# Performance work log

Measured on AMD Instinct MI355X. Metric: run time of the kernel, lower is better.

The kernel has to match this reference:

```python
import jax, jax.numpy as jnp
import numpy as np

B, S, D = 4, 4096, 1024
H, WIN = 16, 256
DK = D // H
NW = S // WIN


def setup_inputs() -> dict:
    key = jax.random.key(0)
    ks = jax.random.split(key, 11)
    mk = lambda k, shape: jax.random.normal(k, shape, dtype=jnp.float32)
    w = lambda k: mk(k, (D, D)) * 0.02  # torch Linear weight [out, in]
    b = lambda k: mk(k, (D,)) * 0.02
    return {
        "query": mk(ks[0], (B, S, D)),
        "key": mk(ks[1], (B, S, D)),
        "value": mk(ks[2], (B, S, D)),
        "Wq": w(ks[3]), "bq": b(ks[4]),
        "Wk": w(ks[5]), "bk": b(ks[6]),
        "Wv": w(ks[7]), "bv": b(ks[8]),
        "Wo": w(ks[9]), "bo": b(ks[10]),
    }


def reference(query, key, value, Wq, bq, Wk, bk, Wv, bv, Wo, bo):
    scale = 1.0 / float(DK) ** 0.5

    def proj(x, Wm, bi):
        y = x @ Wm.T + bi
        return y.reshape(B, S, H, DK).transpose(0, 2, 1, 3).reshape(B, H, NW, WIN, DK)

    q = proj(query, Wq, bq)
    k = proj(key, Wk, bk)
    v = proj(value, Wv, bv)

    scores = jnp.einsum("bhnqd,bhnkd->bhnqk", q, k) * scale
    p_attn = jax.nn.softmax(scores, axis=-1)
    x = jnp.einsum("bhnqk,bhnkd->bhnqd", p_attn, v)

    # merge windows + heads -> [B,S,D], then output projection
    x = x.reshape(B, H, S, DK).transpose(0, 2, 1, 3).reshape(B, S, D)
    return x @ Wo.T + bo
```

## Files before the change

kernel.cpp:

```cpp
#include <hip/hip_runtime.h>
#include <hip/hip_bf16.h>

typedef __attribute__((ext_vector_type(8))) __bf16 bf16x8;
typedef __attribute__((ext_vector_type(4))) float f32x4;

#define DEVI static __device__ __forceinline__


DEVI ushort f2bf(float f) {
  unsigned u = __builtin_bit_cast(unsigned, f);
  return (ushort)((u + 0x7fffu + ((u >> 16) & 1u)) >> 16);
}

union BF8 { unsigned u[4]; bf16x8 v; };

DEVI bf16x8 cvt8(const float* __restrict__ p) {
  const f32x4 a = *(const f32x4*)p;
  const f32x4 b = *(const f32x4*)(p + 4);
  BF8 r;
  asm("v_cvt_pk_bf16_f32 %0, %1, %2" : "=v"(r.u[0]) : "v"(a.x), "v"(a.y));
  asm("v_cvt_pk_bf16_f32 %0, %1, %2" : "=v"(r.u[1]) : "v"(a.z), "v"(a.w));
  asm("v_cvt_pk_bf16_f32 %0, %1, %2" : "=v"(r.u[2]) : "v"(b.x), "v"(b.y));
  asm("v_cvt_pk_bf16_f32 %0, %1, %2" : "=v"(r.u[3]) : "v"(b.z), "v"(b.w));
  return r.v;
}

DEVI bf16x8 cvt8r(f32x4 a, f32x4 b) {
  BF8 r;
  asm("v_cvt_pk_bf16_f32 %0, %1, %2" : "=v"(r.u[0]) : "v"(a.x), "v"(a.y));
  asm("v_cvt_pk_bf16_f32 %0, %1, %2" : "=v"(r.u[1]) : "v"(a.z), "v"(a.w));
  asm("v_cvt_pk_bf16_f32 %0, %1, %2" : "=v"(r.u[2]) : "v"(b.x), "v"(b.y));
  asm("v_cvt_pk_bf16_f32 %0, %1, %2" : "=v"(r.u[3]) : "v"(b.z), "v"(b.w));
  return r.v;
}

DEVI unsigned cvtpk1(float lo, float hi) {
  unsigned r;
  asm("v_cvt_pk_bf16_f32 %0, %1, %2" : "=v"(r) : "v"(lo), "v"(hi));
  return r;
}

DEVI void gload16(const void* g, void* l) {
  __builtin_amdgcn_global_load_lds(
      (const __attribute__((address_space(1))) unsigned*)g,
      (__attribute__((address_space(3))) unsigned*)l, 16, 0, 0);
}

DEVI int xcd_swizzle(int bid, int nwg) {
  return (bid & 7) * (nwg >> 3) + (bid >> 3);
}

DEVI f32x4 mfma16(bf16x8 a, bf16x8 b, f32x4 c) {
  return __builtin_amdgcn_mfma_f32_16x16x32_bf16(a, b, c, 0, 0, 0);
}


__global__ __launch_bounds__(256) void cvt_w(
    const float* __restrict__ wq, const float* __restrict__ wk,
    const float* __restrict__ wv, const float* __restrict__ wo,
    ushort* __restrict__ oq, ushort* __restrict__ ok2,
    ushort* __restrict__ ov, ushort* __restrict__ oo) {
  const int s = blockIdx.x >> 7;
  const int tb = blockIdx.x & 127;
  const float* src = s == 0 ? wq : (s == 1 ? wk : (s == 2 ? wv : wo));
  ushort* dst = s == 0 ? oq : (s == 1 ? ok2 : (s == 2 ? ov : oo));
  const unsigned G = 128 * 256;
  const unsigned t = tb * 256 + threadIdx.x;
#pragma unroll
  for (int j = 0; j < 4; ++j) {
    const size_t i = (size_t)t + (size_t)j * G;
    *(bf16x8*)(dst + i * 8) = cvt8(src + i * 8);
  }
}


template <int OUT>
__global__ __launch_bounds__(512, 2) void gemm_8ph(
    const ushort* __restrict__ A, const ushort* __restrict__ B,
    const float* __restrict__ bias, void* __restrict__ Cp, int N, int K) {
  __shared__ __align__(16) ushort Asm[4][8192];
  __shared__ __align__(16) ushort Bsm[4][8192];
  const int tid = threadIdx.x, lane = tid & 63;
  const int wv = tid >> 6;
  const int wr = wv >> 2, wc = wv & 3;
  const int cc = lane & 15, cr = lane >> 4;
  const int nw = N >> 8;
  const int work = xcd_swizzle(blockIdx.x, gridDim.x);
  const size_t m0 = (size_t)(work / nw) * 256;
  const size_t n0 = (size_t)(work % nw) * 256;

  const ushort *ag[2], *bg[2];
#pragma unroll
  for (int h = 0; h < 2; ++h) {
    const int u = tid + h * 512;
    const int row = u >> 2, slot = u & 3;
    const int gc = (slot ^ ((row >> 1) & 3)) * 8;
    ag[h] = A + (m0 + row) * (size_t)K + gc;
    bg[h] = B + (n0 + row) * (size_t)K + gc;
  }

  auto stageh = [&](int buf, int kt, int h) {
    gload16(ag[h] + kt, &Asm[buf][(tid + h * 512) * 8]);
    gload16(bg[h] + kt, &Bsm[buf][(tid + h * 512) * 8]);
  };

  f32x4 acc[8][4] = {};
  const int nt = K >> 5;

  int aoff[8], boff[4];
#pragma unroll
  for (int m = 0; m < 8; ++m) {
    const int row = wr * 128 + m * 16 + cc;
    aoff[m] = (row * 4 + (cr ^ ((row >> 1) & 3))) * 8;
  }
#pragma unroll
  for (int n = 0; n < 4; ++n) {
    const int row = wc * 64 + n * 16 + cc;
    boff[n] = (row * 4 + (cr ^ ((row >> 1) & 3))) * 8;
  }

#pragma unroll
  for (int p = 0; p < 3; ++p) {
    stageh(p, p << 5, 0);
    stageh(p, p << 5, 1);
  }
  asm volatile("s_waitcnt vmcnt(8)" ::: "memory");
  __builtin_amdgcn_s_barrier();
  asm volatile("" ::: "memory");

  for (int k = 0; k < nt; ++k) {
    const ushort* Ab = Asm[k & 3];
    const ushort* Bb = Bsm[k & 3];
    const int wb = (k + 3) & 3;
    const bool more = (k + 3 < nt);
    bf16x8 bf[4], af[4];

#pragma unroll
    for (int n = 0; n < 4; ++n) bf[n] = *(const bf16x8*)&Bb[boff[n]];
#pragma unroll
    for (int m = 0; m < 4; ++m) af[m] = *(const bf16x8*)&Ab[aoff[m]];
    if (more) stageh(wb, (k + 3) << 5, 0);
    __builtin_amdgcn_s_barrier();
    asm volatile("s_waitcnt lgkmcnt(0)" ::: "memory");
    __builtin_amdgcn_s_setprio(1);
#pragma unroll
    for (int m = 0; m < 4; ++m)
#pragma unroll
      for (int n = 0; n < 4; ++n)
        acc[m][n] = mfma16(af[m], bf[n], acc[m][n]);
    __builtin_amdgcn_s_setprio(0);
    asm volatile("" ::: "memory");
    __builtin_amdgcn_s_barrier();

#pragma unroll
    for (int m = 0; m < 4; ++m) af[m] = *(const bf16x8*)&Ab[aoff[4 + m]];
    if (more) stageh(wb, (k + 3) << 5, 1);
    if (k < nt - 3) {
      asm volatile("s_waitcnt vmcnt(8)" ::: "memory");
    } else if (k == nt - 3) {
      asm volatile("s_waitcnt vmcnt(4)" ::: "memory");
    } else if (k == nt - 2) {
      asm volatile("s_waitcnt vmcnt(0)" ::: "memory");
    }
    __builtin_amdgcn_s_barrier();
    asm volatile("s_waitcnt lgkmcnt(0)" ::: "memory");
    __builtin_amdgcn_s_setprio(1);
#pragma unroll
    for (int m = 0; m < 4; ++m)
#pragma unroll
      for (int n = 0; n < 4; ++n)
        acc[4 + m][n] = mfma16(af[m], bf[n], acc[4 + m][n]);
    __builtin_amdgcn_s_setprio(0);
    asm volatile("" ::: "memory");
    __builtin_amdgcn_s_barrier();
  }

  float bv4[4];
#pragma unroll
  for (int n = 0; n < 4; ++n) bv4[n] = bias[n0 + wc * 64 + n * 16 + cc];

  if constexpr (OUT == 2) {
#pragma unroll
    for (int n = 0; n < 4; ++n) {
      const size_t col = n0 + wc * 64 + n * 16 + cc;
#pragma unroll
      for (int m = 0; m < 8; ++m) {
        const size_t row0 = m0 + wr * 128 + m * 16 + cr * 4;
#pragma unroll
        for (int r = 0; r < 4; ++r)
          ((ushort*)Cp)[col * 16384 + row0 + r] = f2bf(acc[m][n][r] + bv4[n]);
      }
    }
  } else {
#pragma unroll
    for (int m = 0; m < 8; ++m) {
      const size_t row0 = m0 + wr * 128 + m * 16 + cr * 4;
#pragma unroll
      for (int r = 0; r < 4; ++r) {
        const size_t rowoff = (row0 + r) * N;
#pragma unroll
        for (int n = 0; n < 4; ++n) {
          const size_t col = n0 + wc * 64 + n * 16 + cc;
          const float val = acc[m][n][r] + bv4[n];
          if constexpr (OUT == 0)
            ((float*)Cp)[rowoff + col] = val;
          else
            ((ushort*)Cp)[rowoff + col] = f2bf(val);
        }
      }
    }
  }
}


template <int OUT>
__global__ __launch_bounds__(512, 2) void gemm_8ph_f32a(
    const float* __restrict__ A, const ushort* __restrict__ B,
    const float* __restrict__ bias, void* __restrict__ Cp, int N, int K) {
  __shared__ __align__(16) ushort Asm[4][8192];
  __shared__ __align__(16) ushort Bsm[4][8192];
  const int tid = threadIdx.x, lane = tid & 63;
  const int wv = tid >> 6;
  const int wr = wv >> 2, wc = wv & 3;
  const int cc = lane & 15, cr = lane >> 4;
  const int nw = N >> 8;
  const int work = xcd_swizzle(blockIdx.x, gridDim.x);
  const size_t m0 = (size_t)(work / nw) * 256;
  const size_t n0 = (size_t)(work % nw) * 256;

  const float *af0, *af1;
  ushort *al0, *al1;
  {
    const int u0 = tid, r0 = u0 >> 2, s0 = u0 & 3;
    const int u1 = tid + 512, r1 = u1 >> 2, s1 = u1 & 3;
    af0 = A + (m0 + r0) * (size_t)K + (s0 ^ ((r0 >> 1) & 3)) * 8;
    af1 = A + (m0 + r1) * (size_t)K + (s1 ^ ((r1 >> 1) & 3)) * 8;
    al0 = &Asm[0][0] + u0 * 8;
    al1 = &Asm[0][0] + u1 * 8;
  }
  const ushort* bg[2];
#pragma unroll
  for (int h = 0; h < 2; ++h) {
    const int u = tid + h * 512;
    const int row = u >> 2, slot = u & 3;
    bg[h] = B + (n0 + row) * (size_t)K + (slot ^ ((row >> 1) & 3)) * 8;
  }

  f32x4 acc[8][4] = {};
  const int nt = K >> 5;

  int aoff[8], boff[4];
#pragma unroll
  for (int m = 0; m < 8; ++m) {
    const int row = wr * 128 + m * 16 + cc;
    aoff[m] = (row * 4 + (cr ^ ((row >> 1) & 3))) * 8;
  }
#pragma unroll
  for (int n = 0; n < 4; ++n) {
    const int row = wc * 64 + n * 16 + cc;
    boff[n] = (row * 4 + (cr ^ ((row >> 1) & 3))) * 8;
  }

  f32x4 sa0, sa1, sa2, sa3, sb0, sb1, sb2, sb3;
#pragma unroll
  for (int p = 0; p < 2; ++p) {
    const int kt = p << 5;
    sa0 = *(const f32x4*)(af0 + kt);  sa1 = *(const f32x4*)(af0 + kt + 4);
    sa2 = *(const f32x4*)(af1 + kt);  sa3 = *(const f32x4*)(af1 + kt + 4);
    *(bf16x8*)(al0 + p * 8192) = cvt8r(sa0, sa1);
    *(bf16x8*)(al1 + p * 8192) = cvt8r(sa2, sa3);
  }
  sa0 = *(const f32x4*)(af0 + 64);  sa1 = *(const f32x4*)(af0 + 68);
  sa2 = *(const f32x4*)(af1 + 64);  sa3 = *(const f32x4*)(af1 + 68);
#pragma unroll
  for (int p = 0; p < 3; ++p) {
    gload16(bg[0] + (p << 5), &Bsm[p][tid * 8]);
    gload16(bg[1] + (p << 5), &Bsm[p][(tid + 512) * 8]);
  }
  asm volatile("s_waitcnt vmcnt(0) lgkmcnt(0)" ::: "memory");
  __builtin_amdgcn_s_barrier();
  asm volatile("" ::: "memory");

#define F32A_TILE(k, W0, W1, W2, W3, L0, L1, L2, L3)                          \
  {                                                                           \
    const ushort* Ab = Asm[(k) & 3];                                          \
    const ushort* Bb = Bsm[(k) & 3];                                          \
    const int wb = ((k) + 3) & 3;                                             \
    const bool more = ((k) + 3 < nt);                                         \
    bf16x8 bf[4], af[4];                                                      \
    _Pragma("unroll")                                                         \
    for (int n = 0; n < 4; ++n) bf[n] = *(const bf16x8*)&Bb[boff[n]];         \
    _Pragma("unroll")                                                         \
    for (int m = 0; m < 4; ++m) af[m] = *(const bf16x8*)&Ab[aoff[m]];         \
    if ((k) + 2 < nt) {                                                       \
      const int wbuf = ((k) + 2) & 3;                                         \
      *(bf16x8*)(al0 + wbuf * 8192) = cvt8r(W0, W1);                          \
      *(bf16x8*)(al1 + wbuf * 8192) = cvt8r(W2, W3);                          \
    }                                                                         \
    if (more) {                                                               \
      const int kt = ((k) + 3) << 5;                                          \
      L0 = *(const f32x4*)(af0 + kt);  L1 = *(const f32x4*)(af0 + kt + 4);    \
      L2 = *(const f32x4*)(af1 + kt);  L3 = *(const f32x4*)(af1 + kt + 4);    \
      gload16(bg[0] + kt, &Bsm[wb][tid * 8]);                                 \
    }                                                                         \
    if ((k) < nt - 3) {                                                       \
      asm volatile("s_waitcnt vmcnt(17)" ::: "memory");                       \
    } else if ((k) == nt - 3) {                                               \
      asm volatile("s_waitcnt vmcnt(12)" ::: "memory");                       \
    } else if ((k) == nt - 2) {                                               \
      asm volatile("s_waitcnt vmcnt(6)" ::: "memory");                        \
    } else {                                                                  \
      asm volatile("s_waitcnt vmcnt(0)" ::: "memory");                        \
    }                                                                         \
    __builtin_amdgcn_s_barrier();                                             \
    asm volatile("s_waitcnt lgkmcnt(0)" ::: "memory");                        \
    __builtin_amdgcn_s_setprio(1);                                            \
    _Pragma("unroll")                                                         \
    for (int m = 0; m < 4; ++m)                                               \
      _Pragma("unroll")                                                       \
      for (int n = 0; n < 4; ++n) acc[m][n] = mfma16(af[m], bf[n], acc[m][n]);\
    __builtin_amdgcn_s_setprio(0);                                            \
    asm volatile("" ::: "memory");                                            \
    __builtin_amdgcn_s_barrier();                                             \
    _Pragma("unroll")                                                         \
    for (int m = 0; m < 4; ++m) af[m] = *(const bf16x8*)&Ab[aoff[4 + m]];     \
    if (more) gload16(bg[1] + (((k) + 3) << 5), &Bsm[wb][(tid + 512) * 8]);   \
    __builtin_amdgcn_s_barrier();                                             \
    asm volatile("s_waitcnt lgkmcnt(0)" ::: "memory");                        \
    __builtin_amdgcn_s_setprio(1);                                            \
    _Pragma("unroll")                                                         \
    for (int m = 0; m < 4; ++m)                                               \
      _Pragma("unroll")                                                       \
      for (int n = 0; n < 4; ++n)                                             \
        acc[4 + m][n] = mfma16(af[m], bf[n], acc[4 + m][n]);                  \
    __builtin_amdgcn_s_setprio(0);                                            \
    asm volatile("" ::: "memory");                                            \
    __builtin_amdgcn_s_barrier();                                             \
  }

  for (int kk = 0; kk < nt; kk += 2) {
    F32A_TILE(kk, sa0, sa1, sa2, sa3, sb0, sb1, sb2, sb3);
    F32A_TILE(kk + 1, sb0, sb1, sb2, sb3, sa0, sa1, sa2, sa3);
  }
#undef F32A_TILE

  float bv4[4];
#pragma unroll
  for (int n = 0; n < 4; ++n) bv4[n] = bias[n0 + wc * 64 + n * 16 + cc];

  if constexpr (OUT == 2) {
#pragma unroll
    for (int n = 0; n < 4; ++n) {
      const size_t col = n0 + wc * 64 + n * 16 + cc;
#pragma unroll
      for (int m = 0; m < 8; ++m) {
        const size_t row0 = m0 + wr * 128 + m * 16 + cr * 4;
#pragma unroll
        for (int r = 0; r < 4; ++r)
          ((ushort*)Cp)[col * 16384 + row0 + r] = f2bf(acc[m][n][r] + bv4[n]);
      }
    }
  } else {
#pragma unroll
    for (int m = 0; m < 8; ++m) {
      const size_t row0 = m0 + wr * 128 + m * 16 + cr * 4;
#pragma unroll
      for (int r = 0; r < 4; ++r) {
        const size_t rowoff = (row0 + r) * N;
#pragma unroll
        for (int n = 0; n < 4; ++n) {
          const size_t col = n0 + wc * 64 + n * 16 + cc;
          ((ushort*)Cp)[rowoff + col] = f2bf(acc[m][n][r] + bv4[n]);
        }
      }
    }
  }
}


__global__ __launch_bounds__(512, 4) void attn_kernel(
    const ushort* __restrict__ q, const ushort* __restrict__ k,
    const ushort* __restrict__ vt, ushort* __restrict__ x) {
  __shared__ __align__(16) ushort Ks[256 * 64];
  __shared__ __align__(16) ushort Vt[64 * 256];
  const int bid = blockIdx.x;
  const int w = bid & 15, h = (bid >> 4) & 15, b = bid >> 8;
  const int tid = threadIdx.x, lane = tid & 63, wv = tid >> 6;
  const int cc = lane & 15, cr = lane >> 4;
  const size_t base = ((size_t)b * 4096 + (size_t)w * 256) * 1024 + h * 64;
  const size_t vbase = ((size_t)h * 64) * 16384 + (size_t)b * 4096 + w * 256;

  const ushort* qp0 = q + base + (size_t)(wv * 32 + cc) * 1024 + cr * 8;
  const ushort* qp1 = q + base + (size_t)(wv * 32 + 16 + cc) * 1024 + cr * 8;
  const bf16x8 qA0 = *(const bf16x8*)qp0;
  const bf16x8 qA1 = *(const bf16x8*)(qp0 + 32);
  const bf16x8 qB0 = *(const bf16x8*)qp1;
  const bf16x8 qB1 = *(const bf16x8*)(qp1 + 32);

#pragma unroll
  for (int i = 0; i < 4; ++i) {
    const int u = tid + i * 512;
    const int row = u >> 3, slot = u & 7;
    gload16(k + base + (size_t)row * 1024 + ((slot ^ (row & 7)) << 3),
            &Ks[u * 8]);
  }
#pragma unroll
  for (int i = 0; i < 4; ++i) {
    const int u = tid + i * 512;
    const int dk = u >> 5, slot = u & 31;
    gload16(vt + vbase + (size_t)dk * 16384 + (((slot & 24) | ((slot ^ dk) & 7)) << 3),
            &Vt[u * 8]);
  }
  __syncthreads();

  const int s0lane = cc + (2 * (cr & 1)) * 16;
  const int s1lane = s0lane + 16;
  const bool hi = ((cr >> 1) & 1) != 0;

  for (int c = 0; c < 2; ++c) {
    const int qrow0 = wv * 32 + c * 16;
    const bf16x8 qf0 = c == 0 ? qA0 : qB0;
    const bf16x8 qf1 = c == 0 ? qA1 : qB1;

    f32x4 sc[16];
    __builtin_amdgcn_s_setprio(1);
#pragma unroll
    for (int cb = 0; cb < 16; ++cb) {
      const int row = cb * 16 + cc;
      const bf16x8 kb0 = *(const bf16x8*)&Ks[row * 64 + ((cr ^ (row & 7)) << 3)];
      const bf16x8 kb1 =
          *(const bf16x8*)&Ks[row * 64 + (((4 + cr) ^ (row & 7)) << 3)];
      f32x4 z = {0.f, 0.f, 0.f, 0.f};
      z = mfma16(kb0, qf0, z);
      z = mfma16(kb1, qf1, z);
      sc[cb] = z;
    }
    __builtin_amdgcn_s_setprio(0);

    float mx = -1e30f;
#pragma unroll
    for (int cb = 0; cb < 16; ++cb)
#pragma unroll
      for (int r = 0; r < 4; ++r) mx = fmaxf(mx, sc[cb][r]);
    mx = fmaxf(mx, __shfl_xor(mx, 16));
    mx = fmaxf(mx, __shfl_xor(mx, 32));
    float sum = 0.f;
#pragma unroll
    for (int cb = 0; cb < 16; ++cb)
#pragma unroll
      for (int r = 0; r < 4; ++r) {
        const float p = __expf((sc[cb][r] - mx) * 0.125f);
        sc[cb][r] = p;
        sum += p;
      }
    sum += __shfl_xor(sum, 16);
    sum += __shfl_xor(sum, 32);
    const float inv = 1.f / sum;

    f32x4 o[4] = {};
#pragma unroll
    for (int ks = 0; ks < 8; ++ks) {
      const unsigned p00 = cvtpk1(sc[2 * ks][0], sc[2 * ks][1]);
      const unsigned p01 = cvtpk1(sc[2 * ks][2], sc[2 * ks][3]);
      const unsigned p10 = cvtpk1(sc[2 * ks + 1][0], sc[2 * ks + 1][1]);
      const unsigned p11 = cvtpk1(sc[2 * ks + 1][2], sc[2 * ks + 1][3]);
      const unsigned a0 = (unsigned)__shfl((int)p00, s0lane);
      const unsigned b0 = (unsigned)__shfl((int)p10, s0lane);
      const unsigned a1 = (unsigned)__shfl((int)p01, s0lane);
      const unsigned b1 = (unsigned)__shfl((int)p11, s0lane);
      const unsigned a2 = (unsigned)__shfl((int)p00, s1lane);
      const unsigned b2 = (unsigned)__shfl((int)p10, s1lane);
      const unsigned a3 = (unsigned)__shfl((int)p01, s1lane);
      const unsigned b3 = (unsigned)__shfl((int)p11, s1lane);
      BF8 pf;
      pf.u[0] = hi ? b0 : a0;
      pf.u[1] = hi ? b1 : a1;
      pf.u[2] = hi ? b2 : a2;
      pf.u[3] = hi ? b3 : a3;
      __builtin_amdgcn_s_setprio(1);
#pragma unroll
      for (int db = 0; db < 4; ++db) {
        const int row = db * 16 + cc;
        const int gu = ks * 4 + cr;
        const int lu = (gu & 24) | ((gu ^ row) & 7);
        const bf16x8 bv = *(const bf16x8*)&Vt[row * 256 + lu * 8];
        o[db] = mfma16(pf.v, bv, o[db]);
      }
      __builtin_amdgcn_s_setprio(0);
    }

    float invq[4];
#pragma unroll
    for (int r = 0; r < 4; ++r) invq[r] = __shfl(inv, cr * 4 + r);

#pragma unroll
    for (int db = 0; db < 4; ++db)
#pragma unroll
      for (int r = 0; r < 4; ++r) {
        const int qr = qrow0 + cr * 4 + r;
        x[base + (size_t)qr * 1024 + db * 16 + cc] = f2bf(o[db][r] * invq[r]);
      }
  }
}


extern "C" void kernel_launch(void* const* d_in, const int* in_sizes, int n_in,
                              void* d_out, int out_size, void* d_ws, size_t ws_size,
                              hipStream_t stream) {
  const float* query = (const float*)d_in[0];
  const float* key_  = (const float*)d_in[1];
  const float* value = (const float*)d_in[2];
  const float* Wq = (const float*)d_in[3];
  const float* bq = (const float*)d_in[4];
  const float* Wk = (const float*)d_in[5];
  const float* bk = (const float*)d_in[6];
  const float* Wv = (const float*)d_in[7];
  const float* bv = (const float*)d_in[8];
  const float* Wo = (const float*)d_in[9];
  const float* bo = (const float*)d_in[10];
  float* out = (float*)d_out;

  const size_t MN = (size_t)16384 * 1024;
  const size_t WN = (size_t)1024 * 1024;
  ushort* wqb = (ushort*)d_ws;
  ushort* wkb = wqb + WN;
  ushort* wvb = wkb + WN;
  ushort* wob = wvb + WN;
  ushort* qp = wob + WN;
  ushort* kp = qp + MN;
  ushort* vtp = kp + MN;

  const dim3 b256(256), b512(512);
  const dim3 ggrid(256);

  cvt_w<<<dim3(4 * 128), b256, 0, stream>>>(Wq, Wk, Wv, Wo, wqb, wkb, wvb, wob);

  gemm_8ph_f32a<1><<<ggrid, b512, 0, stream>>>(query, wqb, bq, qp, 1024, 1024);
  gemm_8ph_f32a<1><<<ggrid, b512, 0, stream>>>(key_,  wkb, bk, kp, 1024, 1024);
  gemm_8ph_f32a<2><<<ggrid, b512, 0, stream>>>(value, wvb, bv, vtp, 1024, 1024);

  attn_kernel<<<dim3(1024), b512, 0, stream>>>(qp, kp, vtp, qp );

  gemm_8ph<0><<<ggrid, b512, 0, stream>>>(qp, wob, bo, out, 1024, 1024);
}
```

Baseline: 247.5 us.

## Use 128x256 tiles with shallower pipeline for fp32-input QKV projection GEMMs

```diff
diff --git a/kernel.cpp b/kernel.cpp
--- a/kernel.cpp
+++ b/kernel.cpp
@@ -214,29 +214,26 @@
 
 
 template <int OUT>
-__global__ __launch_bounds__(512, 2) void gemm_8ph_f32a(
+__global__ __launch_bounds__(512, 4) void gemm_f32a_hi(
     const float* __restrict__ A, const ushort* __restrict__ B,
     const float* __restrict__ bias, void* __restrict__ Cp, int N, int K) {
-  __shared__ __align__(16) ushort Asm[4][8192];
-  __shared__ __align__(16) ushort Bsm[4][8192];
+  __shared__ __align__(16) ushort Asm2[2][4096];
+  __shared__ __align__(16) ushort Bsm3[3][8192];
   const int tid = threadIdx.x, lane = tid & 63;
   const int wv = tid >> 6;
   const int wr = wv >> 2, wc = wv & 3;
   const int cc = lane & 15, cr = lane >> 4;
   const int nw = N >> 8;
   const int work = xcd_swizzle(blockIdx.x, gridDim.x);
-  const size_t m0 = (size_t)(work / nw) * 256;
+  const size_t m0 = (size_t)(work / nw) * 128;
   const size_t n0 = (size_t)(work % nw) * 256;
 
-  const float *af0, *af1;
-  ushort *al0, *al1;
+  const float* af0;
+  ushort* al0;
   {
-    const int u0 = tid, r0 = u0 >> 2, s0 = u0 & 3;
-    const int u1 = tid + 512, r1 = u1 >> 2, s1 = u1 & 3;
-    af0 = A + (m0 + r0) * (size_t)K + (s0 ^ ((r0 >> 1) & 3)) * 8;
-    af1 = A + (m0 + r1) * (size_t)K + (s1 ^ ((r1 >> 1) & 3)) * 8;
-    al0 = &Asm[0][0] + u0 * 8;
-    al1 = &Asm[0][0] + u1 * 8;
+    const int row = tid >> 2, slot = tid & 3;
+    af0 = A + (m0 + row) * (size_t)K + (slot ^ ((row >> 1) & 3)) * 8;
+    al0 = &Asm2[0][0] + tid * 8;
   }
   const ushort* bg[2];
 #pragma unroll
@@ -246,13 +243,13 @@
     bg[h] = B + (n0 + row) * (size_t)K + (slot ^ ((row >> 1) & 3)) * 8;
   }
 
-  f32x4 acc[8][4] = {};
+  f32x4 acc[4][4] = {};
   const int nt = K >> 5;
 
-  int aoff[8], boff[4];
-#pragma unroll
-  for (int m = 0; m < 8; ++m) {
-    const int row = wr * 128 + m * 16 + cc;
+  int aoff[4], boff[4];
+#pragma unroll
+  for (int m = 0; m < 4; ++m) {
+    const int row = wr * 64 + m * 16 + cc;
     aoff[m] = (row * 4 + (cr ^ ((row >> 1) & 3))) * 8;
   }
 #pragma unroll
@@ -261,54 +258,40 @@
     boff[n] = (row * 4 + (cr ^ ((row >> 1) & 3))) * 8;
   }
 
-  f32x4 sa0, sa1, sa2, sa3, sb0, sb1, sb2, sb3;
+  f32x4 wa0, wa1, la0, la1;
+  wa0 = *(const f32x4*)(af0);      wa1 = *(const f32x4*)(af0 + 4);
+  *(bf16x8*)al0 = cvt8r(wa0, wa1);
+  wa0 = *(const f32x4*)(af0 + 32); wa1 = *(const f32x4*)(af0 + 36);
 #pragma unroll
   for (int p = 0; p < 2; ++p) {
-    const int kt = p << 5;
-    sa0 = *(const f32x4*)(af0 + kt);  sa1 = *(const f32x4*)(af0 + kt + 4);
-    sa2 = *(const f32x4*)(af1 + kt);  sa3 = *(const f32x4*)(af1 + kt + 4);
-    *(bf16x8*)(al0 + p * 8192) = cvt8r(sa0, sa1);
-    *(bf16x8*)(al1 + p * 8192) = cvt8r(sa2, sa3);
-  }
-  sa0 = *(const f32x4*)(af0 + 64);  sa1 = *(const f32x4*)(af0 + 68);
-  sa2 = *(const f32x4*)(af1 + 64);  sa3 = *(const f32x4*)(af1 + 68);
-#pragma unroll
-  for (int p = 0; p < 3; ++p) {
-    gload16(bg[0] + (p << 5), &Bsm[p][tid * 8]);
-    gload16(bg[1] + (p << 5), &Bsm[p][(tid + 512) * 8]);
+    gload16(bg[0] + (p << 5), &Bsm3[p][tid * 8]);
+    gload16(bg[1] + (p << 5), &Bsm3[p][(tid + 512) * 8]);
   }
   asm volatile("s_waitcnt vmcnt(0) lgkmcnt(0)" ::: "memory");
   __builtin_amdgcn_s_barrier();
   asm volatile("" ::: "memory");
 
-#define F32A_TILE(k, W0, W1, W2, W3, L0, L1, L2, L3)                          \
+#define HI_TILE(k, W0, W1, L0, L1)                                            \
   {                                                                           \
-    const ushort* Ab = Asm[(k) & 3];                                          \
-    const ushort* Bb = Bsm[(k) & 3];                                          \
-    const int wb = ((k) + 3) & 3;                                             \
-    const bool more = ((k) + 3 < nt);                                         \
+    const ushort* Ab = &Asm2[(k) & 1][0];                                     \
+    const ushort* Bb = &Bsm3[(k) % 3][0];                                     \
     bf16x8 bf[4], af[4];                                                      \
     _Pragma("unroll")                                                         \
     for (int n = 0; n < 4; ++n) bf[n] = *(const bf16x8*)&Bb[boff[n]];         \
     _Pragma("unroll")                                                         \
     for (int m = 0; m < 4; ++m) af[m] = *(const bf16x8*)&Ab[aoff[m]];         \
+    if ((k) + 1 < nt)                                                         \
+      *(bf16x8*)(al0 + (((k) + 1) & 1) * 4096) = cvt8r(W0, W1);               \
     if ((k) + 2 < nt) {                                                       \
-      const int wbuf = ((k) + 2) & 3;                                         \
-      *(bf16x8*)(al0 + wbuf * 8192) = cvt8r(W0, W1);                          \
-      *(bf16x8*)(al1 + wbuf * 8192) = cvt8r(W2, W3);                          \
+      const int kt = ((k) + 2) << 5;                                          \
+      L0 = *(const f32x4*)(af0 + kt);  L1 = *(const f32x4*)(af0 + kt + 4);    \
+      gload16(bg[0] + kt, &Bsm3[((k) + 2) % 3][tid * 8]);                     \
+      gload16(bg[1] + kt, &Bsm3[((k) + 2) % 3][(tid + 512) * 8]);             \
     }                                                                         \
-    if (more) {                                                               \
-      const int kt = ((k) + 3) << 5;                                          \
-      L0 = *(const f32x4*)(af0 + kt);  L1 = *(const f32x4*)(af0 + kt + 4);    \
-      L2 = *(const f32x4*)(af1 + kt);  L3 = *(const f32x4*)(af1 + kt + 4);    \
-      gload16(bg[0] + kt, &Bsm[wb][tid * 8]);                                 \
-    }                                                                         \
-    if ((k) < nt - 3) {                                                       \
-      asm volatile("s_waitcnt vmcnt(17)" ::: "memory");                       \
-    } else if ((k) == nt - 3) {                                               \
-      asm volatile("s_waitcnt vmcnt(12)" ::: "memory");                       \
+    if ((k) < nt - 2) {                                                       \
+      asm volatile("s_waitcnt vmcnt(8)" ::: "memory");                        \
     } else if ((k) == nt - 2) {                                               \
-      asm volatile("s_waitcnt vmcnt(6)" ::: "memory");                        \
+      asm volatile("s_waitcnt vmcnt(4)" ::: "memory");                        \
     } else {                                                                  \
       asm volatile("s_waitcnt vmcnt(0)" ::: "memory");                        \
     }                                                                         \
@@ -322,27 +305,13 @@
     __builtin_amdgcn_s_setprio(0);                                            \
     asm volatile("" ::: "memory");                                            \
     __builtin_amdgcn_s_barrier();                                             \
-    _Pragma("unroll")                                                         \
-    for (int m = 0; m < 4; ++m) af[m] = *(const bf16x8*)&Ab[aoff[4 + m]];     \
-    if (more) gload16(bg[1] + (((k) + 3) << 5), &Bsm[wb][(tid + 512) * 8]);   \
-    __builtin_amdgcn_s_barrier();                                             \
-    asm volatile("s_waitcnt lgkmcnt(0)" ::: "memory");                        \
-    __builtin_amdgcn_s_setprio(1);                                            \
-    _Pragma("unroll")                                                         \
-    for (int m = 0; m < 4; ++m)                                               \
-      _Pragma("unroll")                                                       \
-      for (int n = 0; n < 4; ++n)                                             \
-        acc[4 + m][n] = mfma16(af[m], bf[n], acc[4 + m][n]);                  \
-    __builtin_amdgcn_s_setprio(0);                                            \
-    asm volatile("" ::: "memory");                                            \
-    __builtin_amdgcn_s_barrier();                                             \
   }
 
   for (int kk = 0; kk < nt; kk += 2) {
-    F32A_TILE(kk, sa0, sa1, sa2, sa3, sb0, sb1, sb2, sb3);
-    F32A_TILE(kk + 1, sb0, sb1, sb2, sb3, sa0, sa1, sa2, sa3);
-  }
-#undef F32A_TILE
+    HI_TILE(kk, wa0, wa1, la0, la1);
+    HI_TILE(kk + 1, la0, la1, wa0, wa1);
+  }
+#undef HI_TILE
 
   float bv4[4];
 #pragma unroll
@@ -353,8 +322,8 @@
     for (int n = 0; n < 4; ++n) {
       const size_t col = n0 + wc * 64 + n * 16 + cc;
 #pragma unroll
-      for (int m = 0; m < 8; ++m) {
-        const size_t row0 = m0 + wr * 128 + m * 16 + cr * 4;
+      for (int m = 0; m < 4; ++m) {
+        const size_t row0 = m0 + wr * 64 + m * 16 + cr * 4;
 #pragma unroll
         for (int r = 0; r < 4; ++r)
           ((ushort*)Cp)[col * 16384 + row0 + r] = f2bf(acc[m][n][r] + bv4[n]);
@@ -362,8 +331,8 @@
     }
   } else {
 #pragma unroll
-    for (int m = 0; m < 8; ++m) {
-      const size_t row0 = m0 + wr * 128 + m * 16 + cr * 4;
+    for (int m = 0; m < 4; ++m) {
+      const size_t row0 = m0 + wr * 64 + m * 16 + cr * 4;
 #pragma unroll
       for (int r = 0; r < 4; ++r) {
         const size_t rowoff = (row0 + r) * N;
@@ -531,15 +500,16 @@
   ushort* vtp = kp + MN;
 
   const dim3 b256(256), b512(512);
-  const dim3 ggrid(256);
+  const dim3 ghi(512);
+  const dim3 g256(256);
 
   cvt_w<<<dim3(4 * 128), b256, 0, stream>>>(Wq, Wk, Wv, Wo, wqb, wkb, wvb, wob);
 
-  gemm_8ph_f32a<1><<<ggrid, b512, 0, stream>>>(query, wqb, bq, qp, 1024, 1024);
-  gemm_8ph_f32a<1><<<ggrid, b512, 0, stream>>>(key_,  wkb, bk, kp, 1024, 1024);
-  gemm_8ph_f32a<2><<<ggrid, b512, 0, stream>>>(value, wvb, bv, vtp, 1024, 1024);
+  gemm_f32a_hi<1><<<ghi, b512, 0, stream>>>(query, wqb, bq, qp, 1024, 1024);
+  gemm_f32a_hi<1><<<ghi, b512, 0, stream>>>(key_,  wkb, bk, kp, 1024, 1024);
+  gemm_f32a_hi<2><<<ghi, b512, 0, stream>>>(value, wvb, bv, vtp, 1024, 1024);
 
   attn_kernel<<<dim3(1024), b512, 0, stream>>>(qp, kp, vtp, qp );
 
-  gemm_8ph<0><<<ggrid, b512, 0, stream>>>(qp, wob, bo, out, 1024, 1024);
-}
+  gemm_8ph<0><<<g256, b512, 0, stream>>>(qp, wob, bo, out, 1024, 1024);
+}
```

After: 265.5 us. 1.07x slower.
